# Kernel optimization log

Hardware: AMD Instinct MI355X
Metric: run time of the kernel (lower is better)

## Reference

```python
import jax, jax.numpy as jnp
import numpy as np

N_ATOMS = 131072
AEV_DIM = 1008
OUT_DIM = 2  # sum(predicted_dim) == len(predicted_properties)
ALPHA = 0.1  # CELU alpha (ANI standard)
# per-element hidden widths for ['H','C','O','N','S','F','Cl']
WIDTHS = [(256, 192, 160), (224, 192, 160), (192, 160, 128), (192, 160, 128),
          (160, 128, 96), (160, 128, 96), (160, 128, 96)]
W1MAX, W2MAX, W3MAX = 256, 192, 160


def _celu(x):
    return jax.nn.celu(x, alpha=ALPHA)


def setup_inputs() -> dict:
    key = jax.random.key(0)
    ks = jax.random.split(key, 2 + 7 * 8)
    species = jax.random.randint(ks[0], (N_ATOMS,), 0, 7)
    aev = jax.random.normal(ks[1], (N_ATOMS, AEV_DIM), dtype=jnp.float32)

    # Padded, stacked per-element weights; only the [:w] blocks are used.
    W1 = np.zeros((7, AEV_DIM, W1MAX), np.float32); b1 = np.zeros((7, W1MAX), np.float32)
    W2 = np.zeros((7, W1MAX, W2MAX), np.float32);  b2 = np.zeros((7, W2MAX), np.float32)
    W3 = np.zeros((7, W2MAX, W3MAX), np.float32);  b3 = np.zeros((7, W3MAX), np.float32)
    Wh = np.zeros((7, W3MAX, OUT_DIM), np.float32); bh = np.zeros((7, OUT_DIM), np.float32)
    for e, (w1, w2, w3) in enumerate(WIDTHS):
        kk = ks[2 + 8 * e: 2 + 8 * (e + 1)]
        W1[e, :, :w1] = np.asarray(jax.random.normal(kk[0], (AEV_DIM, w1))) / np.sqrt(AEV_DIM)
        b1[e, :w1] = np.asarray(jax.random.normal(kk[1], (w1,))) * 0.01
        W2[e, :w1, :w2] = np.asarray(jax.random.normal(kk[2], (w1, w2))) / np.sqrt(w1)
        b2[e, :w2] = np.asarray(jax.random.normal(kk[3], (w2,))) * 0.01
        W3[e, :w2, :w3] = np.asarray(jax.random.normal(kk[4], (w2, w3))) / np.sqrt(w2)
        b3[e, :w3] = np.asarray(jax.random.normal(kk[5], (w3,))) * 0.01
        Wh[e, :w3, :] = np.asarray(jax.random.normal(kk[6], (w3, OUT_DIM))) / np.sqrt(w3)
        bh[e, :] = np.asarray(jax.random.normal(kk[7], (OUT_DIM,))) * 0.01
    return {
        "species": species, "aev": aev,
        "W1": jnp.asarray(W1), "b1": jnp.asarray(b1),
        "W2": jnp.asarray(W2), "b2": jnp.asarray(b2),
        "W3": jnp.asarray(W3), "b3": jnp.asarray(b3),
        "Wh": jnp.asarray(Wh), "bh": jnp.asarray(bh),
    }


def reference(species, aev, W1, b1, W2, b2, W3, b3, Wh, bh):
    # species-routed dispatch -> per-element 3-layer MLP + 2 linear heads -> combine
    out = jnp.zeros((aev.shape[0], OUT_DIM), dtype=aev.dtype)
    for e, (w1, w2, w3) in enumerate(WIDTHS):  # fixed set of 7 structurally distinct experts
        h = _celu(aev @ W1[e, :, :w1] + b1[e, :w1])          # [N, w1]
        h = _celu(h @ W2[e, :w1, :w2] + b2[e, :w2])          # [N, w2]
        h = _celu(h @ W3[e, :w2, :w3] + b3[e, :w3])          # [N, w3]
        y = h @ Wh[e, :w3, :] + bh[e]                        # [N, 2]
        out = out + jnp.where((species == e)[:, None], y, jnp.zeros((), aev.dtype))
    return out
```

## Files before the change

kernel.cpp:

```cpp
#include <hip/hip_runtime.h>

#define NS 7
#define NA 131072
#define AEVD 1008
#define KP1 1024
#define N1 256
#define N2 192
#define N3 160

typedef __attribute__((ext_vector_type(8))) short short8;
typedef __attribute__((ext_vector_type(8))) unsigned short ushortx8;
typedef __attribute__((ext_vector_type(4))) float f32x4;
typedef unsigned short u16;

__device__ __forceinline__ u16 f2bf(float f) {
  unsigned u = __builtin_bit_cast(unsigned, f);
  u += 0x7fffu + ((u >> 16) & 1u);
  return (u16)(u >> 16);
}
__device__ __forceinline__ float bf2f(u16 h) {
  return __builtin_bit_cast(float, ((unsigned)h) << 16);
}
__device__ __forceinline__ float celu_f(float x) {
  return x > 0.f ? x : 0.1f * (__expf(x * 10.f) - 1.f);
}

__global__ void count_kernel(const int* __restrict__ species, int* __restrict__ counts) {
  __shared__ int h[NS];
  if (threadIdx.x < NS) h[threadIdx.x] = 0;
  __syncthreads();
  int i = blockIdx.x * blockDim.x + threadIdx.x;
  if (i < NA) atomicAdd(&h[species[i]], 1);
  __syncthreads();
  if (threadIdx.x < NS) atomicAdd(&counts[threadIdx.x], h[threadIdx.x]);
}

__global__ void scan_kernel(const int* __restrict__ counts, int* __restrict__ offsets,
                            int* __restrict__ cursors, int* __restrict__ blockStart) {
  int off = 0, bs = 0;
  for (int e = 0; e < NS; ++e) {
    offsets[e] = off; cursors[e] = off; blockStart[e] = bs;
    off += counts[e];
    bs += (counts[e] + 63) >> 6;
  }
  offsets[NS] = off; blockStart[NS] = bs;
}

__global__ void scatter_kernel(const int* __restrict__ species, int* __restrict__ cursors,
                               int* __restrict__ idx) {
  __shared__ int h[NS], lb[NS];
  if (threadIdx.x < NS) h[threadIdx.x] = 0;
  __syncthreads();
  int i = blockIdx.x * blockDim.x + threadIdx.x;
  int s = species[i];
  int lpos = atomicAdd(&h[s], 1);
  __syncthreads();
  if (threadIdx.x < NS) lb[threadIdx.x] = atomicAdd(&cursors[threadIdx.x], h[threadIdx.x]);
  __syncthreads();
  idx[lb[s] + lpos] = i;
}

__global__ void convert_w(const float* __restrict__ src, u16* __restrict__ dst,
                          int K, int N, int KP) {
  long total = (long)NS * N * KP;
  for (long i = (long)blockIdx.x * blockDim.x + threadIdx.x; i < total;
       i += (long)gridDim.x * blockDim.x) {
    int kp = (int)(i % KP);
    long t2 = i / KP;
    int n = (int)(t2 % N);
    int e = (int)(t2 / N);
    float v = (kp < K) ? src[((long)e * K + kp) * N + n] : 0.f;
    dst[i] = f2bf(v);
  }
}

#define AP 40
#define WP 40
#define H1P 264
#define H2P 200
#define H3P 168

__global__ __launch_bounds__(256, 2) void ani_fused(
    const int* __restrict__ idx, const int* __restrict__ counts,
    const int* __restrict__ offsets, const int* __restrict__ blockStart,
    const float* __restrict__ aev,
    const u16* __restrict__ W1t, const float* __restrict__ b1,
    const u16* __restrict__ W2t, const float* __restrict__ b2,
    const u16* __restrict__ W3t, const float* __restrict__ b3,
    const u16* __restrict__ Wht, const float* __restrict__ bh,
    float* __restrict__ out) {
  __shared__ __align__(16) u16 R1[12800];
  __shared__ __align__(16) u16 R2[16896];

  int bid = blockIdx.x;
  int total = blockStart[NS];
  if (bid >= total) return;
  int e = 0;
#pragma unroll
  for (int s = 1; s < NS; ++s)
    if (bid >= blockStart[s]) e = s;
  int t = bid - blockStart[e];
  int base = offsets[e] + (t << 6);
  int mcount = counts[e] - (t << 6);
  if (mcount > 64) mcount = 64;

  int tid = threadIdx.x;
  int lane = tid & 63;
  int w = tid >> 6;
  int lr = lane & 15;
  int kg = lane >> 4;

  int arow = tid >> 2;
  int akq = (tid & 3) << 3;
  const float* aevRow = nullptr;
  if (arow < mcount) aevRow = aev + (size_t)idx[base + arow] * AEVD;

  f32x4 acc[4][4] = {};
  const u16* W1base = W1t + (size_t)e * N1 * KP1;
  for (int k0 = 0; k0 < KP1; k0 += 32) {
    {
      float v[8] = {0.f, 0.f, 0.f, 0.f, 0.f, 0.f, 0.f, 0.f};
      if (aevRow != nullptr && (k0 + akq) < AEVD) {
        const float4* p = (const float4*)(aevRow + k0 + akq);
        float4 x = p[0], y = p[1];
        v[0] = x.x; v[1] = x.y; v[2] = x.z; v[3] = x.w;
        v[4] = y.x; v[5] = y.y; v[6] = y.z; v[7] = y.w;
      }
      ushortx8 pk;
#pragma unroll
      for (int j = 0; j < 8; ++j) pk[j] = f2bf(v[j]);
      *(ushortx8*)&R1[arow * AP + akq] = pk;
    }
    {
      const ushortx8* s = (const ushortx8*)(W1base + (size_t)tid * KP1 + k0);
      ushortx8* d = (ushortx8*)&R1[2560 + tid * WP];
      d[0] = s[0]; d[1] = s[1]; d[2] = s[2]; d[3] = s[3];
    }
    __syncthreads();
    short8 af[4];
#pragma unroll
    for (int mi = 0; mi < 4; ++mi)
      af[mi] = *(const short8*)&R1[(mi * 16 + lr) * AP + kg * 8];
#pragma unroll
    for (int ni = 0; ni < 4; ++ni) {
      short8 bf = *(const short8*)&R1[2560 + (w * 64 + ni * 16 + lr) * WP + kg * 8];
#pragma unroll
      for (int mi = 0; mi < 4; ++mi)
        acc[mi][ni] = __builtin_amdgcn_mfma_f32_16x16x32_bf16(af[mi], bf, acc[mi][ni], 0, 0, 0);
    }
    __syncthreads();
  }
#pragma unroll
  for (int ni = 0; ni < 4; ++ni) {
    int col = w * 64 + ni * 16 + lr;
    float bias = b1[e * N1 + col];
#pragma unroll
    for (int mi = 0; mi < 4; ++mi)
#pragma unroll
      for (int r = 0; r < 4; ++r) {
        int row = mi * 16 + kg * 4 + r;
        R2[row * H1P + col] = f2bf(celu_f(acc[mi][ni][r] + bias));
      }
  }
  __syncthreads();

  int mr2 = (w & 1) * 32;
  int nc2 = (w >> 1) * 96;
  f32x4 acc2[2][6] = {};
  const u16* W2base = W2t + (size_t)e * N2 * N1;
  for (int k0 = 0; k0 < N1; k0 += 32) {
    if (tid < N2) {
      const ushortx8* s = (const ushortx8*)(W2base + (size_t)tid * N1 + k0);
      ushortx8* d = (ushortx8*)&R1[tid * WP];
      d[0] = s[0]; d[1] = s[1]; d[2] = s[2]; d[3] = s[3];
    }
    __syncthreads();
    short8 af[2];
#pragma unroll
    for (int mi = 0; mi < 2; ++mi)
      af[mi] = *(const short8*)&R2[(mr2 + mi * 16 + lr) * H1P + k0 + kg * 8];
#pragma unroll
    for (int ni = 0; ni < 6; ++ni) {
      short8 bf = *(const short8*)&R1[(nc2 + ni * 16 + lr) * WP + kg * 8];
#pragma unroll
      for (int mi = 0; mi < 2; ++mi)
        acc2[mi][ni] = __builtin_amdgcn_mfma_f32_16x16x32_bf16(af[mi], bf, acc2[mi][ni], 0, 0, 0);
    }
    __syncthreads();
  }
#pragma unroll
  for (int ni = 0; ni < 6; ++ni) {
    int col = nc2 + ni * 16 + lr;
    float bias = b2[e * N2 + col];
#pragma unroll
    for (int mi = 0; mi < 2; ++mi)
#pragma unroll
      for (int r = 0; r < 4; ++r) {
        int row = mr2 + mi * 16 + kg * 4 + r;
        R2[row * H2P + col] = f2bf(celu_f(acc2[mi][ni][r] + bias));
      }
  }
  __syncthreads();

  int mr3 = (w & 1) * 32;
  int nc3 = (w >> 1) * 80;
  f32x4 acc3[2][5] = {};
  const u16* W3base = W3t + (size_t)e * N3 * N2;
  for (int k0 = 0; k0 < N2; k0 += 32) {
    if (tid < N3) {
      const ushortx8* s = (const ushortx8*)(W3base + (size_t)tid * N2 + k0);
      ushortx8* d = (ushortx8*)&R1[tid * WP];
      d[0] = s[0]; d[1] = s[1]; d[2] = s[2]; d[3] = s[3];
    }
    __syncthreads();
    short8 af[2];
#pragma unroll
    for (int mi = 0; mi < 2; ++mi)
      af[mi] = *(const short8*)&R2[(mr3 + mi * 16 + lr) * H2P + k0 + kg * 8];
#pragma unroll
    for (int ni = 0; ni < 5; ++ni) {
      short8 bf = *(const short8*)&R1[(nc3 + ni * 16 + lr) * WP + kg * 8];
#pragma unroll
      for (int mi = 0; mi < 2; ++mi)
        acc3[mi][ni] = __builtin_amdgcn_mfma_f32_16x16x32_bf16(af[mi], bf, acc3[mi][ni], 0, 0, 0);
    }
    __syncthreads();
  }
  __syncthreads();
#pragma unroll
  for (int ni = 0; ni < 5; ++ni) {
    int col = nc3 + ni * 16 + lr;
    float bias = b3[e * N3 + col];
#pragma unroll
    for (int mi = 0; mi < 2; ++mi)
#pragma unroll
      for (int r = 0; r < 4; ++r) {
        int row = mr3 + mi * 16 + kg * 4 + r;
        R1[row * H3P + col] = f2bf(celu_f(acc3[mi][ni][r] + bias));
      }
  }
  __syncthreads();

  if (tid < 128) {
    int r = tid >> 1, o = tid & 1;
    if (r < mcount) {
      float s = bh[e * 2 + o];
      const u16* wrow = Wht + (e * 2 + o) * N3;
      const u16* hrow = &R1[r * H3P];
#pragma unroll 8
      for (int k = 0; k < N3; ++k) s += bf2f(hrow[k]) * bf2f(wrow[k]);
      out[(size_t)idx[base + r] * 2 + o] = s;
    }
  }
}

extern "C" void kernel_launch(void* const* d_in, const int* in_sizes, int n_in,
                              void* d_out, int out_size, void* d_ws, size_t ws_size,
                              hipStream_t stream) {
  const int* species = (const int*)d_in[0];
  const float* aev = (const float*)d_in[1];
  const float* W1 = (const float*)d_in[2];
  const float* b1 = (const float*)d_in[3];
  const float* W2 = (const float*)d_in[4];
  const float* b2 = (const float*)d_in[5];
  const float* W3 = (const float*)d_in[6];
  const float* b3 = (const float*)d_in[7];
  const float* Wh = (const float*)d_in[8];
  const float* bh = (const float*)d_in[9];
  float* out = (float*)d_out;

  char* p = (char*)d_ws;
  int* counts = (int*)p; p += 32;
  int* offsets = (int*)p; p += 32;
  int* cursors = (int*)p; p += 32;
  int* blockStart = (int*)p; p += 32;
  int* idx = (int*)p; p += (size_t)NA * 4;
  u16* W1t = (u16*)p; p += (size_t)NS * N1 * KP1 * 2;
  u16* W2t = (u16*)p; p += (size_t)NS * N2 * N1 * 2;
  u16* W3t = (u16*)p; p += (size_t)NS * N3 * N2 * 2;
  u16* Wht = (u16*)p; p += (size_t)NS * 2 * N3 * 2;

  hipMemsetAsync(counts, 0, 32, stream);
  count_kernel<<<NA / 256, 256, 0, stream>>>(species, counts);
  scan_kernel<<<1, 1, 0, stream>>>(counts, offsets, cursors, blockStart);
  scatter_kernel<<<NA / 256, 256, 0, stream>>>(species, cursors, idx);

  convert_w<<<2048, 256, 0, stream>>>(W1, W1t, AEVD, N1, KP1);
  convert_w<<<1024, 256, 0, stream>>>(W2, W2t, N1, N2, N1);
  convert_w<<<512, 256, 0, stream>>>(W3, W3t, N2, N3, N2);
  convert_w<<<16, 256, 0, stream>>>(Wh, Wht, N3, 2, N3);

  int maxBlocks = (NA >> 6) + NS;
  ani_fused<<<maxBlocks, 256, 0, stream>>>(idx, counts, offsets, blockStart, aev,
                                           W1t, b1, W2t, b2, W3t, b3, Wht, bh, out);
}
```

Before: 386.8 us.

## Double-buffer AEV tiles and load weights directly into MFMA registers

The layer-1 loop now uses a K step of 64 and double-buffers the converted AEV tile in LDS. The next tile's global loads are issued before the MFMAs and written after them, so one barrier per step replaces two. Weight fragments for all three layers are read straight from global memory (L2-resident bf16) into registers instead of being staged through shared memory, which removes the barriers from layers 2 and 3. The head dot product is spread over all 256 threads with vector loads and a shuffle reduction. The cost is more global weight traffic per wave and higher register pressure.

```diff
diff --git a/kernel.cpp b/kernel.cpp
--- a/kernel.cpp
+++ b/kernel.cpp
@@ -11,6 +11,7 @@
 typedef __attribute__((ext_vector_type(8))) short short8;
 typedef __attribute__((ext_vector_type(8))) unsigned short ushortx8;
 typedef __attribute__((ext_vector_type(4))) float f32x4;
+typedef __attribute__((ext_vector_type(4))) float fvec4;
 typedef unsigned short u16;
 
 __device__ __forceinline__ u16 f2bf(float f) {
@@ -23,6 +24,17 @@
 }
 __device__ __forceinline__ float celu_f(float x) {
   return x > 0.f ? x : 0.1f * (__expf(x * 10.f) - 1.f);
+}
+__device__ __forceinline__ void pack8(fvec4 a, fvec4 b, ushortx8* dst) {
+  ushortx8 p;
+  p[0] = f2bf(a.x); p[1] = f2bf(a.y); p[2] = f2bf(a.z); p[3] = f2bf(a.w);
+  p[4] = f2bf(b.x); p[5] = f2bf(b.y); p[6] = f2bf(b.z); p[7] = f2bf(b.w);
+  *dst = p;
+}
+__device__ __forceinline__ fvec4 ld_aev(const float* row, int k) {
+  if (k < AEVD) return __builtin_nontemporal_load((const fvec4*)(row + k));
+  fvec4 z = {0.f, 0.f, 0.f, 0.f};
+  return z;
 }
 
 __global__ void count_kernel(const int* __restrict__ species, int* __restrict__ counts) {
@@ -74,8 +86,6 @@
   }
 }
 
-#define AP 40
-#define WP 40
 #define H1P 264
 #define H2P 200
 #define H3P 168
@@ -89,12 +99,13 @@
     const u16* __restrict__ W3t, const float* __restrict__ b3,
     const u16* __restrict__ Wht, const float* __restrict__ bh,
     float* __restrict__ out) {
-  __shared__ __align__(16) u16 R1[12800];
-  __shared__ __align__(16) u16 R2[16896];
+  __shared__ __align__(16) u16 AB[2][64 * 72];
+  __shared__ __align__(16) u16 H1[64 * H1P];
+  __shared__ __align__(16) u16 H2[64 * H2P];
+  u16* H3 = H1;
 
   int bid = blockIdx.x;
-  int total = blockStart[NS];
-  if (bid >= total) return;
+  if (bid >= blockStart[NS]) return;
   int e = 0;
 #pragma unroll
   for (int s = 1; s < NS; ++s)
@@ -111,45 +122,60 @@
   int kg = lane >> 4;
 
   int arow = tid >> 2;
-  int akq = (tid & 3) << 3;
-  const float* aevRow = nullptr;
-  if (arow < mcount) aevRow = aev + (size_t)idx[base + arow] * AEVD;
+  int aks = (tid & 3) << 4;
+  int rrow = arow < mcount ? arow : (mcount - 1);
+  const float* aevRow = aev + (size_t)idx[base + rrow] * AEVD;
+
+  {
+    fvec4 v0 = ld_aev(aevRow, aks);
+    fvec4 v1 = ld_aev(aevRow, aks + 4);
+    fvec4 v2 = ld_aev(aevRow, aks + 8);
+    fvec4 v3 = ld_aev(aevRow, aks + 12);
+    pack8(v0, v1, (ushortx8*)&AB[0][arow * 72 + aks]);
+    pack8(v2, v3, (ushortx8*)&AB[0][arow * 72 + aks + 8]);
+  }
+  __syncthreads();
 
   f32x4 acc[4][4] = {};
-  const u16* W1base = W1t + (size_t)e * N1 * KP1;
-  for (int k0 = 0; k0 < KP1; k0 += 32) {
-    {
-      float v[8] = {0.f, 0.f, 0.f, 0.f, 0.f, 0.f, 0.f, 0.f};
-      if (aevRow != nullptr && (k0 + akq) < AEVD) {
-        const float4* p = (const float4*)(aevRow + k0 + akq);
-        float4 x = p[0], y = p[1];
-        v[0] = x.x; v[1] = x.y; v[2] = x.z; v[3] = x.w;
-        v[4] = y.x; v[5] = y.y; v[6] = y.z; v[7] = y.w;
-      }
-      ushortx8 pk;
-#pragma unroll
-      for (int j = 0; j < 8; ++j) pk[j] = f2bf(v[j]);
-      *(ushortx8*)&R1[arow * AP + akq] = pk;
-    }
-    {
-      const ushortx8* s = (const ushortx8*)(W1base + (size_t)tid * KP1 + k0);
-      ushortx8* d = (ushortx8*)&R1[2560 + tid * WP];
-      d[0] = s[0]; d[1] = s[1]; d[2] = s[2]; d[3] = s[3];
+  const u16* Wb1 = W1t + ((size_t)e * N1 + (w * 64 + lr)) * KP1 + kg * 8;
+
+  for (int k0 = 0; k0 < KP1; k0 += 64) {
+    int p = (k0 >> 6) & 1;
+    bool have = (k0 + 64) < KP1;
+    fvec4 v0, v1, v2, v3;
+    if (have) {
+      int kb = k0 + 64 + aks;
+      v0 = ld_aev(aevRow, kb);
+      v1 = ld_aev(aevRow, kb + 4);
+      v2 = ld_aev(aevRow, kb + 8);
+      v3 = ld_aev(aevRow, kb + 12);
+    }
+    short8 bfr[2][4];
+#pragma unroll
+    for (int kk = 0; kk < 2; ++kk)
+#pragma unroll
+      for (int ni = 0; ni < 4; ++ni)
+        bfr[kk][ni] = *(const short8*)(Wb1 + (size_t)ni * 16 * KP1 + k0 + kk * 32);
+    short8 af[2][4];
+#pragma unroll
+    for (int kk = 0; kk < 2; ++kk)
+#pragma unroll
+      for (int mi = 0; mi < 4; ++mi)
+        af[kk][mi] = *(const short8*)&AB[p][(mi * 16 + lr) * 72 + kk * 32 + kg * 8];
+#pragma unroll
+    for (int kk = 0; kk < 2; ++kk)
+#pragma unroll
+      for (int ni = 0; ni < 4; ++ni)
+#pragma unroll
+        for (int mi = 0; mi < 4; ++mi)
+          acc[mi][ni] = __builtin_amdgcn_mfma_f32_16x16x32_bf16(af[kk][mi], bfr[kk][ni], acc[mi][ni], 0, 0, 0);
+    if (have) {
+      pack8(v0, v1, (ushortx8*)&AB[p ^ 1][arow * 72 + aks]);
+      pack8(v2, v3, (ushortx8*)&AB[p ^ 1][arow * 72 + aks + 8]);
     }
     __syncthreads();
-    short8 af[4];
-#pragma unroll
-    for (int mi = 0; mi < 4; ++mi)
-      af[mi] = *(const short8*)&R1[(mi * 16 + lr) * AP + kg * 8];
-#pragma unroll
-    for (int ni = 0; ni < 4; ++ni) {
-      short8 bf = *(const short8*)&R1[2560 + (w * 64 + ni * 16 + lr) * WP + kg * 8];
-#pragma unroll
-      for (int mi = 0; mi < 4; ++mi)
-        acc[mi][ni] = __builtin_amdgcn_mfma_f32_16x16x32_bf16(af[mi], bf, acc[mi][ni], 0, 0, 0);
-    }
-    __syncthreads();
-  }
+  }
+
 #pragma unroll
   for (int ni = 0; ni < 4; ++ni) {
     int col = w * 64 + ni * 16 + lr;
@@ -157,36 +183,25 @@
 #pragma unroll
     for (int mi = 0; mi < 4; ++mi)
 #pragma unroll
-      for (int r = 0; r < 4; ++r) {
-        int row = mi * 16 + kg * 4 + r;
-        R2[row * H1P + col] = f2bf(celu_f(acc[mi][ni][r] + bias));
-      }
+      for (int r = 0; r < 4; ++r)
+        H1[(mi * 16 + kg * 4 + r) * H1P + col] = f2bf(celu_f(acc[mi][ni][r] + bias));
   }
   __syncthreads();
 
   int mr2 = (w & 1) * 32;
   int nc2 = (w >> 1) * 96;
   f32x4 acc2[2][6] = {};
-  const u16* W2base = W2t + (size_t)e * N2 * N1;
+  const u16* Wb2 = W2t + ((size_t)e * N2 + (nc2 + lr)) * N1 + kg * 8;
+#pragma unroll 4
   for (int k0 = 0; k0 < N1; k0 += 32) {
-    if (tid < N2) {
-      const ushortx8* s = (const ushortx8*)(W2base + (size_t)tid * N1 + k0);
-      ushortx8* d = (ushortx8*)&R1[tid * WP];
-      d[0] = s[0]; d[1] = s[1]; d[2] = s[2]; d[3] = s[3];
-    }
-    __syncthreads();
-    short8 af[2];
-#pragma unroll
-    for (int mi = 0; mi < 2; ++mi)
-      af[mi] = *(const short8*)&R2[(mr2 + mi * 16 + lr) * H1P + k0 + kg * 8];
+    short8 a0 = *(const short8*)&H1[(mr2 + lr) * H1P + k0 + kg * 8];
+    short8 a1 = *(const short8*)&H1[(mr2 + 16 + lr) * H1P + k0 + kg * 8];
 #pragma unroll
     for (int ni = 0; ni < 6; ++ni) {
-      short8 bf = *(const short8*)&R1[(nc2 + ni * 16 + lr) * WP + kg * 8];
-#pragma unroll
-      for (int mi = 0; mi < 2; ++mi)
-        acc2[mi][ni] = __builtin_amdgcn_mfma_f32_16x16x32_bf16(af[mi], bf, acc2[mi][ni], 0, 0, 0);
-    }
-    __syncthreads();
+      short8 b = *(const short8*)(Wb2 + (size_t)ni * 16 * N1 + k0);
+      acc2[0][ni] = __builtin_amdgcn_mfma_f32_16x16x32_bf16(a0, b, acc2[0][ni], 0, 0, 0);
+      acc2[1][ni] = __builtin_amdgcn_mfma_f32_16x16x32_bf16(a1, b, acc2[1][ni], 0, 0, 0);
+    }
   }
 #pragma unroll
   for (int ni = 0; ni < 6; ++ni) {
@@ -195,38 +210,26 @@
 #pragma unroll
     for (int mi = 0; mi < 2; ++mi)
 #pragma unroll
-      for (int r = 0; r < 4; ++r) {
-        int row = mr2 + mi * 16 + kg * 4 + r;
-        R2[row * H2P + col] = f2bf(celu_f(acc2[mi][ni][r] + bias));
-      }
+      for (int r = 0; r < 4; ++r)
+        H2[(mr2 + mi * 16 + kg * 4 + r) * H2P + col] = f2bf(celu_f(acc2[mi][ni][r] + bias));
   }
   __syncthreads();
 
   int mr3 = (w & 1) * 32;
   int nc3 = (w >> 1) * 80;
   f32x4 acc3[2][5] = {};
-  const u16* W3base = W3t + (size_t)e * N3 * N2;
+  const u16* Wb3 = W3t + ((size_t)e * N3 + (nc3 + lr)) * N2 + kg * 8;
+#pragma unroll 3
   for (int k0 = 0; k0 < N2; k0 += 32) {
-    if (tid < N3) {
-      const ushortx8* s = (const ushortx8*)(W3base + (size_t)tid * N2 + k0);
-      ushortx8* d = (ushortx8*)&R1[tid * WP];
-      d[0] = s[0]; d[1] = s[1]; d[2] = s[2]; d[3] = s[3];
-    }
-    __syncthreads();
-    short8 af[2];
-#pragma unroll
-    for (int mi = 0; mi < 2; ++mi)
-      af[mi] = *(const short8*)&R2[(mr3 + mi * 16 + lr) * H2P + k0 + kg * 8];
+    short8 a0 = *(const short8*)&H2[(mr3 + lr) * H2P + k0 + kg * 8];
+    short8 a1 = *(const short8*)&H2[(mr3 + 16 + lr) * H2P + k0 + kg * 8];
 #pragma unroll
     for (int ni = 0; ni < 5; ++ni) {
-      short8 bf = *(const short8*)&R1[(nc3 + ni * 16 + lr) * WP + kg * 8];
-#pragma unroll
-      for (int mi = 0; mi < 2; ++mi)
-        acc3[mi][ni] = __builtin_amdgcn_mfma_f32_16x16x32_bf16(af[mi], bf, acc3[mi][ni], 0, 0, 0);
-    }
-    __syncthreads();
-  }
-  __syncthreads();
+      short8 b = *(const short8*)(Wb3 + (size_t)ni * 16 * N2 + k0);
+      acc3[0][ni] = __builtin_amdgcn_mfma_f32_16x16x32_bf16(a0, b, acc3[0][ni], 0, 0, 0);
+      acc3[1][ni] = __builtin_amdgcn_mfma_f32_16x16x32_bf16(a1, b, acc3[1][ni], 0, 0, 0);
+    }
+  }
 #pragma unroll
   for (int ni = 0; ni < 5; ++ni) {
     int col = nc3 + ni * 16 + lr;
@@ -234,23 +237,27 @@
 #pragma unroll
     for (int mi = 0; mi < 2; ++mi)
 #pragma unroll
-      for (int r = 0; r < 4; ++r) {
-        int row = mr3 + mi * 16 + kg * 4 + r;
-        R1[row * H3P + col] = f2bf(celu_f(acc3[mi][ni][r] + bias));
-      }
-  }
-  __syncthreads();
-
-  if (tid < 128) {
-    int r = tid >> 1, o = tid & 1;
-    if (r < mcount) {
-      float s = bh[e * 2 + o];
-      const u16* wrow = Wht + (e * 2 + o) * N3;
-      const u16* hrow = &R1[r * H3P];
-#pragma unroll 8
-      for (int k = 0; k < N3; ++k) s += bf2f(hrow[k]) * bf2f(wrow[k]);
-      out[(size_t)idx[base + r] * 2 + o] = s;
-    }
+      for (int r = 0; r < 4; ++r)
+        H3[(mr3 + mi * 16 + kg * 4 + r) * H3P + col] = f2bf(celu_f(acc3[mi][ni][r] + bias));
+  }
+  __syncthreads();
+
+  {
+    int r = tid >> 2;
+    int o = (tid >> 1) & 1;
+    int kh = tid & 1;
+    float s = 0.f;
+    const u16* wr = Wht + ((size_t)e * 2 + o) * N3 + kh * 80;
+    const u16* hr = &H3[r * H3P + kh * 80];
+#pragma unroll
+    for (int c = 0; c < 10; ++c) {
+      ushortx8 hv = *(const ushortx8*)&hr[c * 8];
+      ushortx8 wv = *(const ushortx8*)&wr[c * 8];
+#pragma unroll
+      for (int j = 0; j < 8; ++j) s += bf2f(hv[j]) * bf2f(wv[j]);
+    }
+    s += __shfl_xor(s, 1);
+    if (kh == 0 && r < mcount) out[(size_t)idx[base + r] * 2 + o] = s + bh[e * 2 + o];
   }
 }
 
@@ -280,7 +287,7 @@
   u16* W3t = (u16*)p; p += (size_t)NS * N3 * N2 * 2;
   u16* Wht = (u16*)p; p += (size_t)NS * 2 * N3 * 2;
 
-  hipMemsetAsync(counts, 0, 32, stream);
+  (void)hipMemsetAsync(counts, 0, 32, stream);
   count_kernel<<<NA / 256, 256, 0, stream>>>(species, counts);
   scan_kernel<<<1, 1, 0, stream>>>(counts, offsets, cursors, blockStart);
   scatter_kernel<<<NA / 256, 256, 0, stream>>>(species, cursors, idx);
```

Result: slower. 470.6 us (+21.7%).
